# Kernel tuning notes

Hardware: AMD Instinct MI355X
Metric: run time of the kernel (lower is better)

## Reference

```python
import jax, jax.numpy as jnp
import numpy as np

D_MODEL = 1024
N_HEADS = 16
D_HEAD = D_MODEL // N_HEADS
D_FF = 4096
SEQ_LEN = 2048
BATCH = 4


def setup_inputs() -> dict:
    key = jax.random.key(0)
    ks = jax.random.split(key, 6)
    s = lambda fan_in: 1.0 / np.sqrt(fan_in)
    x = jax.random.normal(ks[0], (BATCH, SEQ_LEN, D_MODEL), dtype=jnp.float32)
    # weights stored [in, out] (transpose of torch Linear weight)
    w_qkv = jax.random.uniform(ks[1], (D_MODEL, 3 * D_MODEL), jnp.float32, -s(D_MODEL), s(D_MODEL))
    w_out = jax.random.uniform(ks[2], (D_MODEL, D_MODEL), jnp.float32, -s(D_MODEL), s(D_MODEL))
    w_ff1 = jax.random.uniform(ks[3], (D_MODEL, D_FF), jnp.float32, -s(D_MODEL), s(D_MODEL))
    w_ff2 = jax.random.uniform(ks[4], (D_FF, D_MODEL), jnp.float32, -s(D_FF), s(D_FF))
    return {"x": x, "w_qkv": w_qkv, "w_out": w_out, "w_ff1": w_ff1, "w_ff2": w_ff2}


def reference(x, w_qkv, w_out, w_ff1, w_ff2):
    B, Tlen, C = x.shape
    # ln1/ln2 are Identity (use_layer_norm=False)
    qkv = (x @ w_qkv).reshape(B, Tlen, 3, N_HEADS, D_HEAD)
    qkv = jnp.transpose(qkv, (2, 0, 3, 1, 4))  # [3, B, H, T, Dh]
    q, k, v = qkv[0], qkv[1], qkv[2]
    scale = D_HEAD ** (-0.5)
    attn = jnp.einsum("bhqd,bhkd->bhqk", q, k) * scale  # [B,H,T,T]
    causal = jnp.triu(jnp.ones((Tlen, Tlen), dtype=bool), k=1)
    attn = jnp.where(causal, -jnp.inf, attn)
    attn = jax.nn.softmax(attn, axis=-1)
    out = jnp.einsum("bhqk,bhkd->bhqd", attn, v)  # [B,H,T,Dh]
    out = jnp.transpose(out, (0, 2, 1, 3)).reshape(B, Tlen, C)
    x = x + out @ w_out
    h = jax.nn.gelu(x @ w_ff1, approximate=False)  # torch F.gelu default = exact erf
    x = x + h @ w_ff2
    return x
```

## Files before the change

### kernel.cpp

```cpp
#include <hip/hip_runtime.h>

typedef __bf16 bf16;
typedef __bf16 bf16x8 __attribute__((ext_vector_type(8)));
typedef __bf16 bf16x4 __attribute__((ext_vector_type(4)));
typedef float f32x4 __attribute__((ext_vector_type(4)));
typedef unsigned int u32;
typedef unsigned short u16;

#define MFMA_BF16 __builtin_amdgcn_mfma_f32_16x16x32_bf16

#define GLOAD_LDS(g, l)                                        \
  __builtin_amdgcn_global_load_lds(                            \
      (__attribute__((address_space(1))) void*)(g),            \
      (__attribute__((address_space(3))) void*)(l), 16, 0, 0)

__global__ void cvt_f32_bf16(const float* __restrict__ in, bf16* __restrict__ out, int n) {
  int i = (blockIdx.x * blockDim.x + threadIdx.x) * 4;
  if (i >= n) return;
  float4 v = *(const float4*)(in + i);
  bf16x4 o;
  o[0] = (bf16)v.x; o[1] = (bf16)v.y; o[2] = (bf16)v.z; o[3] = (bf16)v.w;
  *(bf16x4*)(out + i) = o;
}

__global__ void transpose_w(const float* __restrict__ w, bf16* __restrict__ wt, int K, int N) {
  __shared__ float tile[32][33];
  int n0 = blockIdx.x * 32, k0 = blockIdx.y * 32;
  int t = threadIdx.x;
  int c = t & 31, r = t >> 5;
#pragma unroll
  for (int i = 0; i < 4; i++)
    tile[r + i * 8][c] = w[(size_t)(k0 + r + i * 8) * N + n0 + c];
  __syncthreads();
#pragma unroll
  for (int i = 0; i < 4; i++)
    wt[(size_t)(n0 + r + i * 8) * K + k0 + c] = (bf16)tile[c][r + i * 8];
}

__device__ inline float gelu_exact(float x) {
  return 0.5f * x * (1.0f + erff(x * 0.70710678118654752f));
}

template <int MODE, int WTM>
__global__ __launch_bounds__(256, (WTM == 128) ? 2 : 4) void gemm_bt(
    const bf16* __restrict__ A, const bf16* __restrict__ Bt,
    bf16* __restrict__ outb, float* __restrict__ outf,
    const float* __restrict__ residf, const bf16* __restrict__ residb,
    int K, int N) {
  constexpr int BM = WTM * 2;
  constexpr int MR = WTM / 16;
  __shared__ __align__(16) bf16 As[2][BM * 32];
  __shared__ __align__(16) bf16 Bs[2][128 * 32];
  const int tid = threadIdx.x;
  const int lane = tid & 63, w = tid >> 6;
  const int g = lane >> 4, l15 = lane & 15;
  const int wm = w >> 1, wn = w & 1;

  constexpr int MT = 8192 / BM;
  const int NT = N >> 7;
  const int nsupN = NT >> 2;
  const int cpx = (int)gridDim.x >> 3;
  const int widx = ((int)blockIdx.x & 7) * cpx + ((int)blockIdx.x >> 3);
  const int s = widx >> 4, r4 = widx & 15;
  const int sm = s / nsupN, sn = s - sm * nsupN;
  const int m0 = (sm * 4 + (r4 & 3)) * BM;
  const int n0 = (sn * 4 + (r4 >> 2)) * 128;

  f32x4 acc[MR][4] = {};

  const int srow = tid >> 2;
  const int schunk = (tid & 3) ^ ((tid >> 3) & 3);
  const char* gA = (const char*)A;
  const char* gB = (const char*)Bt;
  const size_t aOff = ((size_t)(m0 + srow) * K + schunk * 8) * 2;
  const size_t bOff = ((size_t)(n0 + srow) * K + schunk * 8) * 2;

  auto stage = [&](int kt, int slot) {
    const size_t kb = (size_t)kt * 64;
#pragma unroll
    for (int i = 0; i < BM / 64; i++)
      GLOAD_LDS(gA + aOff + (size_t)(i * 64) * K * 2 + kb,
                &As[slot][(i * 64 + w * 16) * 32]);
#pragma unroll
    for (int i = 0; i < 2; i++)
      GLOAD_LDS(gB + bOff + (size_t)(i * 64) * K * 2 + kb,
                &Bs[slot][(i * 64 + w * 16) * 32]);
  };

  const int rsw = (g ^ ((l15 >> 1) & 3)) << 4;
  const int rdA = (wm * WTM + l15) * 64 + rsw;
  const int rdB = (wn * 64 + l15) * 64 + rsw;

  const int T = K >> 5;
  stage(0, 0);

  int slot = 0;
  for (int t = 0; t < T; ++t) {
    __syncthreads();
    if (t + 1 < T) stage(t + 1, slot ^ 1);
    const char* pA = (const char*)As[slot];
    const char* pB = (const char*)Bs[slot];
    bf16x8 a[MR], b[4];
#pragma unroll
    for (int mi = 0; mi < MR; mi++) a[mi] = *(const bf16x8*)(pA + rdA + mi * 1024);
#pragma unroll
    for (int ni = 0; ni < 4; ni++) b[ni] = *(const bf16x8*)(pB + rdB + ni * 1024);
    __builtin_amdgcn_s_setprio(1);
#pragma unroll
    for (int mi = 0; mi < MR; mi++)
#pragma unroll
      for (int ni = 0; ni < 4; ni++)
        acc[mi][ni] = MFMA_BF16(a[mi], b[ni], acc[mi][ni], 0, 0, 0);
    __builtin_amdgcn_s_setprio(0);
    slot ^= 1;
  }

  const int row_base = m0 + wm * WTM;
  const int col_base = n0 + wn * 64 + l15;
#pragma unroll
  for (int mi = 0; mi < MR; mi++)
#pragma unroll
    for (int ni = 0; ni < 4; ni++) {
      const int c = col_base + ni * 16;
#pragma unroll
      for (int r = 0; r < 4; r++) {
        const int row = row_base + mi * 16 + 4 * g + r;
        const size_t idx = (size_t)row * N + c;
        float v = acc[mi][ni][r];
        if constexpr (MODE == 0) {
          outb[idx] = (bf16)v;
        } else if constexpr (MODE == 1) {
          outb[idx] = (bf16)(v + residf[idx]);
        } else if constexpr (MODE == 2) {
          outb[idx] = (bf16)gelu_exact(v);
        } else {
          outf[idx] = v + (float)residb[idx];
        }
      }
    }
}

__global__ __launch_bounds__(512, 2) void attn_fwd(const bf16* __restrict__ qkv,
                                                   bf16* __restrict__ O) {
  __shared__ __align__(16) char Kl[2][64 * 128];
  __shared__ __align__(16) char Vt[2][64 * 128];
  const int tid = threadIdx.x;
  const int lane = tid & 63, w = tid >> 6;
  const int g = lane >> 4, l15 = lane & 15;
  const int bh = blockIdx.x;
  const int bx = blockIdx.y;
  const int b = bh >> 4, hh = bh & 15;
  const size_t tokbase = (size_t)b * 2048;

  const bf16* kbase = qkv + tokbase * 3072 + 1024 + hh * 64;
  const bf16* vbase = qkv + tokbase * 3072 + 2048 + hh * 64;
  const int kperm = 8 * (l15 >> 2) + (l15 & 3);

  const bool vstage = tid < 256;
  const int t2 = tid & 255;
  const int vrg = t2 >> 4, vds = (t2 & 15) * 4;
  const int krow = t2 >> 2, ksl = t2 & 3;
  const int kswzr = (krow & 3) | ((krow & 8) >> 1);

  union U4 { ushort4 v; u16 a[4]; };
  U4 vr[4];
  uint4 kpr0, kpr1;

  auto prefetch = [&](int k0n) {
    if (vstage) {
#pragma unroll
      for (int i4 = 0; i4 < 4; i4++)
        vr[i4].v = *(const ushort4*)(vbase + (size_t)(k0n + 4 * vrg + i4) * 3072 + vds);
    } else {
      const bf16* kp = kbase + (size_t)(k0n + krow) * 3072 + 8 * ksl;
      kpr0 = *(const uint4*)(kp);
      kpr1 = *(const uint4*)(kp + 32);
    }
  };

  prefetch(0);
  int cur = 0;

  for (int half = 0; half < 2; half++) {
    const int xT = half ? (15 - bx) : bx;
    const int q0 = xT * 128;
    const int qw0 = q0 + 16 * w;
    const int qi = qw0 + l15;
    const int kend = q0 + 128;

    const bf16* qptr = qkv + (tokbase + qw0 + l15) * 3072 + hh * 64 + 8 * g;
    const bf16x8 qf0 = *(const bf16x8*)(qptr);
    const bf16x8 qf1 = *(const bf16x8*)(qptr + 32);

    f32x4 ot[4] = {};
    float m_i = -INFINITY, l_i = 0.0f;

    for (int k0 = 0; k0 < kend; k0 += 64) {
      char* Kc = Kl[cur];
      char* Vc = Vt[cur];
      if (vstage) {
#pragma unroll
        for (int dj = 0; dj < 4; dj++) {
          const int d = vds + dj;
          u32 lo = (u32)vr[0].a[dj] | ((u32)vr[1].a[dj] << 16);
          u32 hi = (u32)vr[2].a[dj] | ((u32)vr[3].a[dj] << 16);
          const int boff = d * 128 + ((((vrg >> 1) ^ ((d >> 1) & 7)) << 4)) + ((vrg & 1) << 3);
          *(uint2*)(Vc + boff) = make_uint2(lo, hi);
        }
      } else {
        *(uint4*)(Kc + krow * 128 + ((ksl ^ kswzr) << 4)) = kpr0;
        *(uint4*)(Kc + krow * 128 + (((ksl | 4) ^ kswzr) << 4)) = kpr1;
      }
      __syncthreads();

      const int k0n = (k0 + 64 < kend) ? k0 + 64 : 0;
      prefetch(k0n);

      if (k0 <= qw0 + 15) {
        const bool lastT = (k0 + 63 > qw0);
        const int npair = lastT ? (((qw0 + 15 - k0) >> 5) + 1) : 2;

        f32x4 st[4];
#pragma unroll
        for (int ip = 0; ip < 2; ip++)
          if (ip < npair) {
#pragma unroll
            for (int h2 = 0; h2 < 2; h2++) {
              const int kr = 32 * ip + 4 * h2 + kperm;
              const int swzk = (kr & 3) | ((kr & 8) >> 1);
              const char* kro = Kc + kr * 128;
              bf16x8 ka = *(const bf16x8*)(kro + ((g ^ swzk) << 4));
              bf16x8 kb = *(const bf16x8*)(kro + (((g | 4) ^ swzk) << 4));
              f32x4 z = {};
              z = MFMA_BF16(ka, qf0, z, 0, 0, 0);
              st[2 * ip + h2] = MFMA_BF16(kb, qf1, z, 0, 0, 0);
            }
          }

        float p[4][4];
        float mt = -INFINITY;
#pragma unroll
        for (int ip = 0; ip < 2; ip++)
          if (ip < npair) {
#pragma unroll
            for (int h2 = 0; h2 < 2; h2++)
#pragma unroll
              for (int r = 0; r < 4; r++) {
                const int kk = k0 + 32 * ip + 8 * g + 4 * h2 + r;
                float v = (float)st[2 * ip + h2][r] * 0.125f;
                if (lastT && kk > qi) v = -INFINITY;
                p[2 * ip + h2][r] = v;
                mt = fmaxf(mt, v);
              }
          }

        if (!__all(mt - m_i <= 8.0f)) {
          mt = fmaxf(mt, __shfl_xor(mt, 16, 64));
          mt = fmaxf(mt, __shfl_xor(mt, 32, 64));
          const float m_new = fmaxf(m_i, mt);
          const float alpha = __expf(m_i - m_new);
          l_i *= alpha;
#pragma unroll
          for (int dt = 0; dt < 4; dt++)
#pragma unroll
            for (int r = 0; r < 4; r++) ot[dt][r] *= alpha;
          m_i = m_new;
        }
        float s = 0.0f;
#pragma unroll
        for (int ip = 0; ip < 2; ip++)
          if (ip < npair) {
#pragma unroll
            for (int h2 = 0; h2 < 2; h2++)
#pragma unroll
              for (int r = 0; r < 4; r++) {
                float e = __expf(p[2 * ip + h2][r] - m_i);
                p[2 * ip + h2][r] = e;
                s += e;
              }
          }
        l_i += s;

#pragma unroll
        for (int ip = 0; ip < 2; ip++)
          if (ip < npair) {
            bf16x8 pf;
#pragma unroll
            for (int h2 = 0; h2 < 2; h2++)
#pragma unroll
              for (int r = 0; r < 4; r++) pf[4 * h2 + r] = (bf16)p[2 * ip + h2][r];
#pragma unroll
            for (int dt = 0; dt < 4; dt++) {
              const bf16x8 vf = *(const bf16x8*)(
                  Vc + (dt * 16 + l15) * 128 + (((4 * ip + g) ^ (l15 >> 1)) << 4));
              ot[dt] = MFMA_BF16(vf, pf, ot[dt], 0, 0, 0);
            }
          }
      }
      cur ^= 1;
    }

    l_i += __shfl_xor(l_i, 16, 64);
    l_i += __shfl_xor(l_i, 32, 64);
    const float inv = 1.0f / l_i;
    bf16* obase = O + (tokbase + qw0 + l15) * 1024 + hh * 64;
#pragma unroll
    for (int dt = 0; dt < 4; dt++) {
      bf16x4 ov;
#pragma unroll
      for (int r = 0; r < 4; r++) ov[r] = (bf16)(ot[dt][r] * inv);
      *(bf16x4*)(obase + dt * 16 + 4 * g) = ov;
    }
  }
}

extern "C" void kernel_launch(void* const* d_in, const int* in_sizes, int n_in,
                              void* d_out, int out_size, void* d_ws, size_t ws_size,
                              hipStream_t stream) {
  const float* x = (const float*)d_in[0];
  const float* w_qkv = (const float*)d_in[1];
  const float* w_out = (const float*)d_in[2];
  const float* w_ff1 = (const float*)d_in[3];
  const float* w_ff2 = (const float*)d_in[4];
  float* out = (float*)d_out;

  char* ws = (char*)d_ws;
  size_t off = 0;
  auto alloc = [&](size_t bytes) {
    void* p = ws + off;
    off += (bytes + 255) & ~(size_t)255;
    return p;
  };
  const size_t M = 8192;
  bf16* X16   = (bf16*)alloc(M * 1024 * 2);
  bf16* WqkvT = (bf16*)alloc(3072ull * 1024 * 2);
  bf16* WoutT = (bf16*)alloc(1024ull * 1024 * 2);
  bf16* Wff1T = (bf16*)alloc(4096ull * 1024 * 2);
  bf16* Wff2T = (bf16*)alloc(1024ull * 4096 * 2);
  bf16* QKV   = (bf16*)alloc(M * 3072 * 2);
  bf16* Obuf  = (bf16*)alloc(M * 1024 * 2);
  bf16* x1b   = (bf16*)alloc(M * 1024 * 2);
  bf16* Hbuf  = (bf16*)alloc(M * 4096 * 2);

  cvt_f32_bf16<<<8192, 256, 0, stream>>>(x, X16, 8192 * 1024);
  transpose_w<<<dim3(3072 / 32, 1024 / 32), 256, 0, stream>>>(w_qkv, WqkvT, 1024, 3072);
  transpose_w<<<dim3(1024 / 32, 1024 / 32), 256, 0, stream>>>(w_out, WoutT, 1024, 1024);
  transpose_w<<<dim3(4096 / 32, 1024 / 32), 256, 0, stream>>>(w_ff1, Wff1T, 1024, 4096);
  transpose_w<<<dim3(1024 / 32, 4096 / 32), 256, 0, stream>>>(w_ff2, Wff2T, 4096, 1024);

  gemm_bt<0, 128><<<32 * 24, 256, 0, stream>>>(X16, WqkvT, QKV, nullptr, nullptr, nullptr, 1024, 3072);
  attn_fwd<<<dim3(64, 8), 512, 0, stream>>>(QKV, Obuf);
  gemm_bt<1, 64><<<64 * 8, 256, 0, stream>>>(Obuf, WoutT, x1b, nullptr, x, nullptr, 1024, 1024);
  gemm_bt<2, 128><<<32 * 32, 256, 0, stream>>>(x1b, Wff1T, Hbuf, nullptr, nullptr, nullptr, 1024, 4096);
  gemm_bt<3, 64><<<64 * 8, 256, 0, stream>>>(Hbuf, Wff2T, nullptr, out, nullptr, x1b, 4096, 1024);
}
```

Measured before the change: 383.4 us.

## Load GEMM B operand directly from global into registers, bypassing LDS

The B tile is no longer staged through shared memory. Each lane now loads its B fragments straight from global memory into registers, double-buffered across two k-steps, and the main loop is unrolled by two so the buffers can alternate. This frees LDS capacity and removes the LDS writes and reads for B. In exchange, each B element is fetched from global memory by both M-waves with no sharing, the global loads are narrow strided 16-byte accesses, and the unrolled loop assumes an even number of k-steps.

```diff
diff --git a/kernel.cpp b/kernel.cpp
--- a/kernel.cpp
+++ b/kernel.cpp
@@ -50,13 +50,11 @@
   constexpr int BM = WTM * 2;
   constexpr int MR = WTM / 16;
   __shared__ __align__(16) bf16 As[2][BM * 32];
-  __shared__ __align__(16) bf16 Bs[2][128 * 32];
   const int tid = threadIdx.x;
   const int lane = tid & 63, w = tid >> 6;
   const int g = lane >> 4, l15 = lane & 15;
   const int wm = w >> 1, wn = w & 1;
 
-  constexpr int MT = 8192 / BM;
   const int NT = N >> 7;
   const int nsupN = NT >> 2;
   const int cpx = (int)gridDim.x >> 3;
@@ -71,9 +69,7 @@
   const int srow = tid >> 2;
   const int schunk = (tid & 3) ^ ((tid >> 3) & 3);
   const char* gA = (const char*)A;
-  const char* gB = (const char*)Bt;
   const size_t aOff = ((size_t)(m0 + srow) * K + schunk * 8) * 2;
-  const size_t bOff = ((size_t)(n0 + srow) * K + schunk * 8) * 2;
 
   auto stage = [&](int kt, int slot) {
     const size_t kb = (size_t)kt * 64;
@@ -81,37 +77,62 @@
     for (int i = 0; i < BM / 64; i++)
       GLOAD_LDS(gA + aOff + (size_t)(i * 64) * K * 2 + kb,
                 &As[slot][(i * 64 + w * 16) * 32]);
-#pragma unroll
-    for (int i = 0; i < 2; i++)
-      GLOAD_LDS(gB + bOff + (size_t)(i * 64) * K * 2 + kb,
-                &Bs[slot][(i * 64 + w * 16) * 32]);
   };
+
+  const bf16* bG = Bt + (size_t)(n0 + wn * 64 + l15) * K + 8 * g;
 
   const int rsw = (g ^ ((l15 >> 1) & 3)) << 4;
   const int rdA = (wm * WTM + l15) * 64 + rsw;
-  const int rdB = (wn * 64 + l15) * 64 + rsw;
 
   const int T = K >> 5;
+  bf16x8 b0[4], b1[4];
   stage(0, 0);
+#pragma unroll
+  for (int ni = 0; ni < 4; ni++) b0[ni] = *(const bf16x8*)(bG + (size_t)(ni * 16) * K);
 
   int slot = 0;
-  for (int t = 0; t < T; ++t) {
+  for (int t = 0; t < T; t += 2) {
     __syncthreads();
-    if (t + 1 < T) stage(t + 1, slot ^ 1);
-    const char* pA = (const char*)As[slot];
-    const char* pB = (const char*)Bs[slot];
-    bf16x8 a[MR], b[4];
-#pragma unroll
-    for (int mi = 0; mi < MR; mi++) a[mi] = *(const bf16x8*)(pA + rdA + mi * 1024);
-#pragma unroll
-    for (int ni = 0; ni < 4; ni++) b[ni] = *(const bf16x8*)(pB + rdB + ni * 1024);
-    __builtin_amdgcn_s_setprio(1);
-#pragma unroll
-    for (int mi = 0; mi < MR; mi++)
+    if (t + 1 < T) {
+      stage(t + 1, slot ^ 1);
 #pragma unroll
       for (int ni = 0; ni < 4; ni++)
-        acc[mi][ni] = MFMA_BF16(a[mi], b[ni], acc[mi][ni], 0, 0, 0);
-    __builtin_amdgcn_s_setprio(0);
+        b1[ni] = *(const bf16x8*)(bG + (size_t)(ni * 16) * K + (t + 1) * 32);
+    }
+    {
+      const char* pA = (const char*)As[slot];
+      bf16x8 a[MR];
+#pragma unroll
+      for (int mi = 0; mi < MR; mi++) a[mi] = *(const bf16x8*)(pA + rdA + mi * 1024);
+      __builtin_amdgcn_s_setprio(1);
+#pragma unroll
+      for (int mi = 0; mi < MR; mi++)
+#pragma unroll
+        for (int ni = 0; ni < 4; ni++)
+          acc[mi][ni] = MFMA_BF16(a[mi], b0[ni], acc[mi][ni], 0, 0, 0);
+      __builtin_amdgcn_s_setprio(0);
+    }
+    slot ^= 1;
+    __syncthreads();
+    if (t + 2 < T) {
+      stage(t + 2, slot ^ 1);
+#pragma unroll
+      for (int ni = 0; ni < 4; ni++)
+        b0[ni] = *(const bf16x8*)(bG + (size_t)(ni * 16) * K + (t + 2) * 32);
+    }
+    {
+      const char* pA = (const char*)As[slot];
+      bf16x8 a[MR];
+#pragma unroll
+      for (int mi = 0; mi < MR; mi++) a[mi] = *(const bf16x8*)(pA + rdA + mi * 1024);
+      __builtin_amdgcn_s_setprio(1);
+#pragma unroll
+      for (int mi = 0; mi < MR; mi++)
+#pragma unroll
+        for (int ni = 0; ni < 4; ni++)
+          acc[mi][ni] = MFMA_BF16(a[mi], b1[ni], acc[mi][ni], 0, 0, 0);
+      __builtin_amdgcn_s_setprio(0);
+    }
     slot ^= 1;
   }
 
```

Result: slower. 504.3 us (+31.5%).

## Fuse paired causal query tiles into one K/V pass sharing staged tiles

Applied to the files above, without the earlier changes.

The attention kernel previously handled its two query tiles (bx and 15-bx) in two sequential passes, each restaging K/V into LDS. Now a single loop over keys up to the high tile's end stages each K/V tile once and applies it to both query tiles, each with its own online-softmax state. This removes the duplicated global loads, LDS stores and barriers for the shared prefix of keys. In exchange it doubles the live accumulator registers, which may lower occupancy.

```diff
diff --git a/kernel.cpp b/kernel.cpp
--- a/kernel.cpp
+++ b/kernel.cpp
@@ -56,7 +56,6 @@
   const int g = lane >> 4, l15 = lane & 15;
   const int wm = w >> 1, wn = w & 1;
 
-  constexpr int MT = 8192 / BM;
   const int NT = N >> 7;
   const int nsupN = NT >> 2;
   const int cpx = (int)gridDim.x >> 3;
@@ -178,137 +177,156 @@
     }
   };
 
+  const int q0l = bx * 128, q0h = (15 - bx) * 128;
+  const int qw0l = q0l + 16 * w, qw0h = q0h + 16 * w;
+  const int qil = qw0l + l15, qih = qw0h + l15;
+  const int kend = q0h + 128;
+
+  const bf16* qpl = qkv + (tokbase + qw0l + l15) * 3072 + hh * 64 + 8 * g;
+  const bf16x8 qfl0 = *(const bf16x8*)(qpl);
+  const bf16x8 qfl1 = *(const bf16x8*)(qpl + 32);
+  const bf16* qph = qkv + (tokbase + qw0h + l15) * 3072 + hh * 64 + 8 * g;
+  const bf16x8 qfh0 = *(const bf16x8*)(qph);
+  const bf16x8 qfh1 = *(const bf16x8*)(qph + 32);
+
+  f32x4 otl[4] = {}, oth[4] = {};
+  float ml = -INFINITY, ll = 0.0f, mh = -INFINITY, lh = 0.0f;
+
   prefetch(0);
   int cur = 0;
 
-  for (int half = 0; half < 2; half++) {
-    const int xT = half ? (15 - bx) : bx;
-    const int q0 = xT * 128;
-    const int qw0 = q0 + 16 * w;
-    const int qi = qw0 + l15;
-    const int kend = q0 + 128;
-
-    const bf16* qptr = qkv + (tokbase + qw0 + l15) * 3072 + hh * 64 + 8 * g;
-    const bf16x8 qf0 = *(const bf16x8*)(qptr);
-    const bf16x8 qf1 = *(const bf16x8*)(qptr + 32);
-
-    f32x4 ot[4] = {};
-    float m_i = -INFINITY, l_i = 0.0f;
-
-    for (int k0 = 0; k0 < kend; k0 += 64) {
-      char* Kc = Kl[cur];
-      char* Vc = Vt[cur];
-      if (vstage) {
-#pragma unroll
-        for (int dj = 0; dj < 4; dj++) {
-          const int d = vds + dj;
-          u32 lo = (u32)vr[0].a[dj] | ((u32)vr[1].a[dj] << 16);
-          u32 hi = (u32)vr[2].a[dj] | ((u32)vr[3].a[dj] << 16);
-          const int boff = d * 128 + ((((vrg >> 1) ^ ((d >> 1) & 7)) << 4)) + ((vrg & 1) << 3);
-          *(uint2*)(Vc + boff) = make_uint2(lo, hi);
-        }
-      } else {
-        *(uint4*)(Kc + krow * 128 + ((ksl ^ kswzr) << 4)) = kpr0;
-        *(uint4*)(Kc + krow * 128 + (((ksl | 4) ^ kswzr) << 4)) = kpr1;
+  for (int k0 = 0; k0 < kend; k0 += 64) {
+    char* Kc = Kl[cur];
+    char* Vc = Vt[cur];
+    if (vstage) {
+#pragma unroll
+      for (int dj = 0; dj < 4; dj++) {
+        const int d = vds + dj;
+        u32 lo = (u32)vr[0].a[dj] | ((u32)vr[1].a[dj] << 16);
+        u32 hi = (u32)vr[2].a[dj] | ((u32)vr[3].a[dj] << 16);
+        const int boff = d * 128 + ((((vrg >> 1) ^ ((d >> 1) & 7)) << 4)) + ((vrg & 1) << 3);
+        *(uint2*)(Vc + boff) = make_uint2(lo, hi);
       }
-      __syncthreads();
-
-      const int k0n = (k0 + 64 < kend) ? k0 + 64 : 0;
-      prefetch(k0n);
-
-      if (k0 <= qw0 + 15) {
-        const bool lastT = (k0 + 63 > qw0);
-        const int npair = lastT ? (((qw0 + 15 - k0) >> 5) + 1) : 2;
-
-        f32x4 st[4];
-#pragma unroll
-        for (int ip = 0; ip < 2; ip++)
-          if (ip < npair) {
-#pragma unroll
-            for (int h2 = 0; h2 < 2; h2++) {
-              const int kr = 32 * ip + 4 * h2 + kperm;
-              const int swzk = (kr & 3) | ((kr & 8) >> 1);
-              const char* kro = Kc + kr * 128;
-              bf16x8 ka = *(const bf16x8*)(kro + ((g ^ swzk) << 4));
-              bf16x8 kb = *(const bf16x8*)(kro + (((g | 4) ^ swzk) << 4));
-              f32x4 z = {};
-              z = MFMA_BF16(ka, qf0, z, 0, 0, 0);
-              st[2 * ip + h2] = MFMA_BF16(kb, qf1, z, 0, 0, 0);
+    } else {
+      *(uint4*)(Kc + krow * 128 + ((ksl ^ kswzr) << 4)) = kpr0;
+      *(uint4*)(Kc + krow * 128 + (((ksl | 4) ^ kswzr) << 4)) = kpr1;
+    }
+    __syncthreads();
+
+    const int k0n = (k0 + 64 < kend) ? k0 + 64 : 0;
+    prefetch(k0n);
+
+    auto tile_step = [&](const bf16x8& qa, const bf16x8& qb, f32x4* ot,
+                         float& m_i, float& l_i, int qw0, int qi) {
+      const bool lastT = (k0 + 63 > qw0);
+      const int npair = lastT ? (((qw0 + 15 - k0) >> 5) + 1) : 2;
+
+      f32x4 st[4];
+#pragma unroll
+      for (int ip = 0; ip < 2; ip++)
+        if (ip < npair) {
+#pragma unroll
+          for (int h2 = 0; h2 < 2; h2++) {
+            const int kr = 32 * ip + 4 * h2 + kperm;
+            const int swzk = (kr & 3) | ((kr & 8) >> 1);
+            const char* kro = Kc + kr * 128;
+            bf16x8 ka = *(const bf16x8*)(kro + ((g ^ swzk) << 4));
+            bf16x8 kb = *(const bf16x8*)(kro + (((g | 4) ^ swzk) << 4));
+            f32x4 z = {};
+            z = MFMA_BF16(ka, qa, z, 0, 0, 0);
+            st[2 * ip + h2] = MFMA_BF16(kb, qb, z, 0, 0, 0);
+          }
+        }
+
+      float p[4][4];
+      float mt = -INFINITY;
+#pragma unroll
+      for (int ip = 0; ip < 2; ip++)
+        if (ip < npair) {
+#pragma unroll
+          for (int h2 = 0; h2 < 2; h2++)
+#pragma unroll
+            for (int r = 0; r < 4; r++) {
+              const int kk = k0 + 32 * ip + 8 * g + 4 * h2 + r;
+              float v = (float)st[2 * ip + h2][r] * 0.125f;
+              if (lastT && kk > qi) v = -INFINITY;
+              p[2 * ip + h2][r] = v;
+              mt = fmaxf(mt, v);
             }
+        }
+
+      if (!__all(mt - m_i <= 8.0f)) {
+        mt = fmaxf(mt, __shfl_xor(mt, 16, 64));
+        mt = fmaxf(mt, __shfl_xor(mt, 32, 64));
+        const float m_new = fmaxf(m_i, mt);
+        const float alpha = __expf(m_i - m_new);
+        l_i *= alpha;
+#pragma unroll
+        for (int dt = 0; dt < 4; dt++)
+#pragma unroll
+          for (int r = 0; r < 4; r++) ot[dt][r] *= alpha;
+        m_i = m_new;
+      }
+      float s = 0.0f;
+#pragma unroll
+      for (int ip = 0; ip < 2; ip++)
+        if (ip < npair) {
+#pragma unroll
+          for (int h2 = 0; h2 < 2; h2++)
+#pragma unroll
+            for (int r = 0; r < 4; r++) {
+              float e = __expf(p[2 * ip + h2][r] - m_i);
+              p[2 * ip + h2][r] = e;
+              s += e;
+            }
+        }
+      l_i += s;
+
+#pragma unroll
+      for (int ip = 0; ip < 2; ip++)
+        if (ip < npair) {
+          bf16x8 pf;
+#pragma unroll
+          for (int h2 = 0; h2 < 2; h2++)
+#pragma unroll
+            for (int r = 0; r < 4; r++) pf[4 * h2 + r] = (bf16)p[2 * ip + h2][r];
+#pragma unroll
+          for (int dt = 0; dt < 4; dt++) {
+            const bf16x8 vf = *(const bf16x8*)(
+                Vc + (dt * 16 + l15) * 128 + (((4 * ip + g) ^ (l15 >> 1)) << 4));
+            ot[dt] = MFMA_BF16(vf, pf, ot[dt], 0, 0, 0);
           }
-
-        float p[4][4];
-        float mt = -INFINITY;
-#pragma unroll
-        for (int ip = 0; ip < 2; ip++)
-          if (ip < npair) {
-#pragma unroll
-            for (int h2 = 0; h2 < 2; h2++)
-#pragma unroll
-              for (int r = 0; r < 4; r++) {
-                const int kk = k0 + 32 * ip + 8 * g + 4 * h2 + r;
-                float v = (float)st[2 * ip + h2][r] * 0.125f;
-                if (lastT && kk > qi) v = -INFINITY;
-                p[2 * ip + h2][r] = v;
-                mt = fmaxf(mt, v);
-              }
-          }
-
-        if (!__all(mt - m_i <= 8.0f)) {
-          mt = fmaxf(mt, __shfl_xor(mt, 16, 64));
-          mt = fmaxf(mt, __shfl_xor(mt, 32, 64));
-          const float m_new = fmaxf(m_i, mt);
-          const float alpha = __expf(m_i - m_new);
-          l_i *= alpha;
-#pragma unroll
-          for (int dt = 0; dt < 4; dt++)
-#pragma unroll
-            for (int r = 0; r < 4; r++) ot[dt][r] *= alpha;
-          m_i = m_new;
-        }
-        float s = 0.0f;
-#pragma unroll
-        for (int ip = 0; ip < 2; ip++)
-          if (ip < npair) {
-#pragma unroll
-            for (int h2 = 0; h2 < 2; h2++)
-#pragma unroll
-              for (int r = 0; r < 4; r++) {
-                float e = __expf(p[2 * ip + h2][r] - m_i);
-                p[2 * ip + h2][r] = e;
-                s += e;
-              }
-          }
-        l_i += s;
-
-#pragma unroll
-        for (int ip = 0; ip < 2; ip++)
-          if (ip < npair) {
-            bf16x8 pf;
-#pragma unroll
-            for (int h2 = 0; h2 < 2; h2++)
-#pragma unroll
-              for (int r = 0; r < 4; r++) pf[4 * h2 + r] = (bf16)p[2 * ip + h2][r];
-#pragma unroll
-            for (int dt = 0; dt < 4; dt++) {
-              const bf16x8 vf = *(const bf16x8*)(
-                  Vc + (dt * 16 + l15) * 128 + (((4 * ip + g) ^ (l15 >> 1)) << 4));
-              ot[dt] = MFMA_BF16(vf, pf, ot[dt], 0, 0, 0);
-            }
-          }
-      }
-      cur ^= 1;
-    }
-
-    l_i += __shfl_xor(l_i, 16, 64);
-    l_i += __shfl_xor(l_i, 32, 64);
-    const float inv = 1.0f / l_i;
-    bf16* obase = O + (tokbase + qw0 + l15) * 1024 + hh * 64;
+        }
+    };
+
+    if (k0 <= qw0l + 15) tile_step(qfl0, qfl1, otl, ml, ll, qw0l, qil);
+    if (k0 <= qw0h + 15) tile_step(qfh0, qfh1, oth, mh, lh, qw0h, qih);
+    cur ^= 1;
+  }
+
+  {
+    float l = ll + __shfl_xor(ll, 16, 64);
+    l += __shfl_xor(l, 32, 64);
+    const float inv = 1.0f / l;
+    bf16* obase = O + (tokbase + qw0l + l15) * 1024 + hh * 64;
 #pragma unroll
     for (int dt = 0; dt < 4; dt++) {
       bf16x4 ov;
 #pragma unroll
-      for (int r = 0; r < 4; r++) ov[r] = (bf16)(ot[dt][r] * inv);
+      for (int r = 0; r < 4; r++) ov[r] = (bf16)(otl[dt][r] * inv);
+      *(bf16x4*)(obase + dt * 16 + 4 * g) = ov;
+    }
+  }
+  {
+    float l = lh + __shfl_xor(lh, 16, 64);
+    l += __shfl_xor(l, 32, 64);
+    const float inv = 1.0f / l;
+    bf16* obase = O + (tokbase + qw0h + l15) * 1024 + hh * 64;
+#pragma unroll
+    for (int dt = 0; dt < 4; dt++) {
+      bf16x4 ov;
+#pragma unroll
+      for (int r = 0; r < 4; r++) ov[r] = (bf16)(oth[dt][r] * inv);
       *(bf16x4*)(obase + dt * 16 + 4 * g) = ov;
     }
   }
```

Result: slower. 404.8 us (+5.6%).

## Load K tiles via direct global-to-LDS and fold softmax scale into QKV GEMM

Applied to the files above, without the earlier changes.

K tiles in the attention kernel are now loaded straight into LDS with global_load_lds by all 512 threads, instead of being staged through registers by half the block and written with ds_write. This frees registers and cuts LDS write instructions. The 1/sqrt(d) scale moves into the QKV GEMM epilogue, applied to the Q columns before the bf16 store, so the per-element multiply in attention goes away. The causal mask is also split into a separate branch that runs only on diagonal tiles. Scaling before rounding to bf16 changes numerics slightly, and correctness now depends on the async LDS load being complete before the barrier.

```diff
diff --git a/kernel.cpp b/kernel.cpp
--- a/kernel.cpp
+++ b/kernel.cpp
@@ -56,7 +56,6 @@
   const int g = lane >> 4, l15 = lane & 15;
   const int wm = w >> 1, wn = w & 1;
 
-  constexpr int MT = 8192 / BM;
   const int NT = N >> 7;
   const int nsupN = NT >> 2;
   const int cpx = (int)gridDim.x >> 3;
@@ -115,6 +114,7 @@
     slot ^= 1;
   }
 
+  const float qsc = (MODE == 0 && n0 < 1024) ? 0.125f : 1.0f;
   const int row_base = m0 + wm * WTM;
   const int col_base = n0 + wn * 64 + l15;
 #pragma unroll
@@ -128,7 +128,7 @@
         const size_t idx = (size_t)row * N + c;
         float v = acc[mi][ni][r];
         if constexpr (MODE == 0) {
-          outb[idx] = (bf16)v;
+          outb[idx] = (bf16)(v * qsc);
         } else if constexpr (MODE == 1) {
           outb[idx] = (bf16)(v + residf[idx]);
         } else if constexpr (MODE == 2) {
@@ -156,29 +156,30 @@
   const bf16* vbase = qkv + tokbase * 3072 + 2048 + hh * 64;
   const int kperm = 8 * (l15 >> 2) + (l15 & 3);
 
+  const int kr8 = tid >> 3, kc = tid & 7;
+  const int kswz = (kr8 & 3) | ((kr8 & 8) >> 1);
+  const bf16* kSrc = kbase + (size_t)kr8 * 3072 + 8 * (kc ^ kswz);
+
   const bool vstage = tid < 256;
   const int t2 = tid & 255;
   const int vrg = t2 >> 4, vds = (t2 & 15) * 4;
-  const int krow = t2 >> 2, ksl = t2 & 3;
-  const int kswzr = (krow & 3) | ((krow & 8) >> 1);
 
   union U4 { ushort4 v; u16 a[4]; };
   U4 vr[4];
-  uint4 kpr0, kpr1;
-
-  auto prefetch = [&](int k0n) {
+
+  auto prefetchV = [&](int k0n) {
     if (vstage) {
 #pragma unroll
       for (int i4 = 0; i4 < 4; i4++)
         vr[i4].v = *(const ushort4*)(vbase + (size_t)(k0n + 4 * vrg + i4) * 3072 + vds);
-    } else {
-      const bf16* kp = kbase + (size_t)(k0n + krow) * 3072 + 8 * ksl;
-      kpr0 = *(const uint4*)(kp);
-      kpr1 = *(const uint4*)(kp + 32);
     }
   };
-
-  prefetch(0);
+  auto gloadK = [&](int k0n, int buf) {
+    GLOAD_LDS(kSrc + (size_t)k0n * 3072, Kl[buf] + w * 1024);
+  };
+
+  prefetchV(0);
+  gloadK(0, 0);
   int cur = 0;
 
   for (int half = 0; half < 2; half++) {
@@ -203,18 +204,16 @@
         for (int dj = 0; dj < 4; dj++) {
           const int d = vds + dj;
           u32 lo = (u32)vr[0].a[dj] | ((u32)vr[1].a[dj] << 16);
-          u32 hi = (u32)vr[2].a[dj] | ((u32)vr[3].a[dj] << 16);
+          u32 hi2 = (u32)vr[2].a[dj] | ((u32)vr[3].a[dj] << 16);
           const int boff = d * 128 + ((((vrg >> 1) ^ ((d >> 1) & 7)) << 4)) + ((vrg & 1) << 3);
-          *(uint2*)(Vc + boff) = make_uint2(lo, hi);
+          *(uint2*)(Vc + boff) = make_uint2(lo, hi2);
         }
-      } else {
-        *(uint4*)(Kc + krow * 128 + ((ksl ^ kswzr) << 4)) = kpr0;
-        *(uint4*)(Kc + krow * 128 + (((ksl | 4) ^ kswzr) << 4)) = kpr1;
       }
       __syncthreads();
 
       const int k0n = (k0 + 64 < kend) ? k0 + 64 : 0;
-      prefetch(k0n);
+      prefetchV(k0n);
+      gloadK(k0n, cur ^ 1);
 
       if (k0 <= qw0 + 15) {
         const bool lastT = (k0 + 63 > qw0);
@@ -238,21 +237,34 @@
           }
 
         float p[4][4];
+#pragma unroll
+        for (int ip = 0; ip < 2; ip++)
+          if (ip < npair)
+#pragma unroll
+            for (int h2 = 0; h2 < 2; h2++)
+#pragma unroll
+              for (int r = 0; r < 4; r++)
+                p[2 * ip + h2][r] = (float)st[2 * ip + h2][r];
+        if (lastT) {
+#pragma unroll
+          for (int ip = 0; ip < 2; ip++)
+            if (ip < npair)
+#pragma unroll
+              for (int h2 = 0; h2 < 2; h2++)
+#pragma unroll
+                for (int r = 0; r < 4; r++) {
+                  const int kk = k0 + 32 * ip + 8 * g + 4 * h2 + r;
+                  if (kk > qi) p[2 * ip + h2][r] = -INFINITY;
+                }
+        }
         float mt = -INFINITY;
 #pragma unroll
         for (int ip = 0; ip < 2; ip++)
-          if (ip < npair) {
+          if (ip < npair)
 #pragma unroll
             for (int h2 = 0; h2 < 2; h2++)
 #pragma unroll
-              for (int r = 0; r < 4; r++) {
-                const int kk = k0 + 32 * ip + 8 * g + 4 * h2 + r;
-                float v = (float)st[2 * ip + h2][r] * 0.125f;
-                if (lastT && kk > qi) v = -INFINITY;
-                p[2 * ip + h2][r] = v;
-                mt = fmaxf(mt, v);
-              }
-          }
+              for (int r = 0; r < 4; r++) mt = fmaxf(mt, p[2 * ip + h2][r]);
 
         if (!__all(mt - m_i <= 8.0f)) {
           mt = fmaxf(mt, __shfl_xor(mt, 16, 64));
@@ -266,7 +278,7 @@
             for (int r = 0; r < 4; r++) ot[dt][r] *= alpha;
           m_i = m_new;
         }
-        float s = 0.0f;
+        float sum = 0.0f;
 #pragma unroll
         for (int ip = 0; ip < 2; ip++)
           if (ip < npair) {
@@ -276,10 +288,10 @@
               for (int r = 0; r < 4; r++) {
                 float e = __expf(p[2 * ip + h2][r] - m_i);
                 p[2 * ip + h2][r] = e;
-                s += e;
+                sum += e;
               }
           }
-        l_i += s;
+        l_i += sum;
 
 #pragma unroll
         for (int ip = 0; ip < 2; ip++)
```

Result: no change. 380.4 us (-0.8%).
